# Kernel optimization log

Hardware: AMD Instinct MI355X
Metric: run time of the kernel (lower is better)

The kernel has to match this reference:

```python
import jax, jax.numpy as jnp
import numpy as np

E = 512   # embed_dim
H = 8     # num_heads
D = E // H  # head_dim


def setup_inputs() -> dict:
    key = jax.random.key(0)
    ks = jax.random.split(key, 13)
    B, Nq, Nk = 4, 2048, 2048
    query = jax.random.normal(ks[0], (B, Nq, E), dtype=jnp.float32)
    key_t = jax.random.normal(ks[1], (B, Nk, E), dtype=jnp.float32)
    value = jax.random.normal(ks[2], (B, Nk, E), dtype=jnp.float32)
    geometry_mask = jax.random.bernoulli(ks[3], 0.5, (B, Nq, Nk))  # True = keep
    s = 1.0 / np.sqrt(E)
    Wq = jax.random.normal(ks[4], (E, E), dtype=jnp.float32) * s
    bq = jax.random.normal(ks[5], (E,), dtype=jnp.float32) * 0.01
    Wk = jax.random.normal(ks[6], (E, E), dtype=jnp.float32) * s
    bk = jax.random.normal(ks[7], (E,), dtype=jnp.float32) * 0.01
    Wv = jax.random.normal(ks[8], (E, E), dtype=jnp.float32) * s
    bv = jax.random.normal(ks[9], (E,), dtype=jnp.float32) * 0.01
    Wo = jax.random.normal(ks[10], (E, E), dtype=jnp.float32) * s
    bo = jax.random.normal(ks[11], (E,), dtype=jnp.float32) * 0.01
    return {"query": query, "key": key_t, "value": value,
            "geometry_mask": geometry_mask,
            "Wq": Wq, "bq": bq, "Wk": Wk, "bk": bk,
            "Wv": Wv, "bv": bv, "Wo": Wo, "bo": bo}


def reference(query, key, value, geometry_mask, Wq, bq, Wk, bk, Wv, bv, Wo, bo):
    B, Nq, _ = query.shape
    Nk = key.shape[1]
    scale = D ** -0.5
    # projections -> (B, H, N, D)
    Q = (query @ Wq + bq).reshape(B, Nq, H, D).transpose(0, 2, 1, 3)
    K = (key @ Wk + bk).reshape(B, Nk, H, D).transpose(0, 2, 1, 3)
    V = (value @ Wv + bv).reshape(B, Nk, H, D).transpose(0, 2, 1, 3)
    scores = jnp.einsum('bhqd,bhkd->bhqk', Q, K) * scale
    mask = geometry_mask[:, None, :, :]  # (B,1,Nq,Nk), True = keep
    scores = jnp.where(mask, scores, -jnp.inf)
    attn = jax.nn.softmax(scores, axis=-1)  # dropout p=0 (eval)
    out = jnp.einsum('bhqk,bhkd->bhqd', attn, V)
    out = out.transpose(0, 2, 1, 3).reshape(B, Nq, E)
    return out @ Wo + bo
```

## Files before the change

### kernel.cpp

```cpp
#include <hip/hip_runtime.h>
#include <stdint.h>


typedef __attribute__((ext_vector_type(8))) short bf16x8;
typedef __attribute__((ext_vector_type(4))) float f32x4;

#define SCLQ 0.18033688011112042f

static __device__ __forceinline__ unsigned short f2bf(float f) {
    union { float f; unsigned u; } x; x.f = f;
    unsigned r = x.u + 0x7fffu + ((x.u >> 16) & 1u);
    return (unsigned short)(r >> 16);
}

static __device__ __forceinline__ f32x4 mfma16(bf16x8 a, bf16x8 b, f32x4 c) {
    return __builtin_amdgcn_mfma_f32_16x16x32_bf16(a, b, c, 0, 0, 0);
}

#define GLOAD_LDS16(g, l)                                                            \
    __builtin_amdgcn_global_load_lds((const __attribute__((address_space(1))) void*)(g), \
                                     (__attribute__((address_space(3))) void*)(l), 16, 0, 0)


__global__ __launch_bounds__(256) void cvt_x_kernel(
    const float* __restrict__ xq, const float* __restrict__ xk, const float* __restrict__ xv,
    short* __restrict__ oq, short* __restrict__ ok, short* __restrict__ ov)
{
    const float* src = (blockIdx.y == 0) ? xq : (blockIdx.y == 1) ? xk : xv;
    short* dst = (blockIdx.y == 0) ? oq : (blockIdx.y == 1) ? ok : ov;
    size_t i = (size_t)blockIdx.x * 256 + threadIdx.x;
    float4 v = ((const float4*)src)[i];
    short4 o;
    o.x = (short)f2bf(v.x); o.y = (short)f2bf(v.y);
    o.z = (short)f2bf(v.z); o.w = (short)f2bf(v.w);
    ((short4*)dst)[i] = o;
}

__global__ __launch_bounds__(256) void cvt_wt_kernel(
    const float* __restrict__ Wq, const float* __restrict__ Wk,
    const float* __restrict__ Wv, const float* __restrict__ Wo,
    short* __restrict__ WqT, short* __restrict__ WkT,
    short* __restrict__ WvT, short* __restrict__ WoT)
{
    int z = blockIdx.y;
    const float* W = (z == 0) ? Wq : (z == 1) ? Wk : (z == 2) ? Wv : Wo;
    short* WT = (z == 0) ? WqT : (z == 1) ? WkT : (z == 2) ? WvT : WoT;
    int t = blockIdx.x * 256 + threadIdx.x;
    int n = t & 511;
    int k0 = (t >> 9) * 8;
    union { short s[8]; int4 v; } u;
#pragma unroll
    for (int j = 0; j < 8; ++j) u.s[j] = (short)f2bf(W[(size_t)(k0 + j) * 512 + n]);
    *(int4*)(WT + (size_t)n * 512 + k0) = u.v;
}

__global__ __launch_bounds__(256) void pack_mask_kernel(
    const int* __restrict__ mask, unsigned long long* __restrict__ mp)
{
    int lane = threadIdx.x & 63;
    int row = blockIdx.x * 4 + (threadIdx.x >> 6);
    const int* mrow = mask + (size_t)row * 2048;
#pragma unroll 4
    for (int w = 0; w < 32; ++w) {
        unsigned long long bits = __ballot(mrow[w * 64 + lane] != 0);
        if (lane == 0) mp[(size_t)row * 32 + w] = bits;
    }
}

static __device__ __forceinline__ void gemm_body(
    const short* __restrict__ A, const short* __restrict__ BT,
    const float* __restrict__ bias, void* __restrict__ Cout, int mode,
    char* lds, int bx, int by)
{
    const int tid = threadIdx.x;
    const int lane = tid & 63;
    const int wid = tid >> 6;
    const int l15 = lane & 15, l4 = lane >> 4;
    const int m0 = by * 128;
    const int n0 = bx * 128;
    const int wr = wid >> 1, wc = wid & 1;

    f32x4 zero = {0.f, 0.f, 0.f, 0.f};
    f32x4 acc[4][4];
#pragma unroll
    for (int i = 0; i < 4; ++i)
#pragma unroll
        for (int j = 0; j < 4; ++j) acc[i][j] = zero;

    char* Alds = lds;
    char* Blds = lds + 16384;

    for (int t = 0; t < 8; ++t) {
        const int k0 = t * 64;
#pragma unroll
        for (int s = 0; s < 4; ++s) {
            int p = s * 256 + tid;
            int r = p >> 3, c = p & 7;
            GLOAD_LDS16(A + (size_t)(m0 + r) * 512 + k0 + 8 * (c ^ (r & 7)),
                        Alds + s * 4096 + wid * 1024);
            GLOAD_LDS16(BT + (size_t)(n0 + r) * 512 + k0 + 8 * (c ^ (r & 7)),
                        Blds + s * 4096 + wid * 1024);
        }
        __syncthreads();
#pragma unroll
        for (int ks = 0; ks < 2; ++ks) {
            bf16x8 af[4], bfr[4];
#pragma unroll
            for (int mb = 0; mb < 4; ++mb) {
                int row = wr * 64 + mb * 16 + l15;
                af[mb] = *(const bf16x8*)(Alds + row * 128 +
                                          ((ks * 64 + l4 * 16) ^ ((row & 7) << 4)));
            }
#pragma unroll
            for (int nb = 0; nb < 4; ++nb) {
                int row = wc * 64 + nb * 16 + l15;
                bfr[nb] = *(const bf16x8*)(Blds + row * 128 +
                                           ((ks * 64 + l4 * 16) ^ ((row & 7) << 4)));
            }
#pragma unroll
            for (int mb = 0; mb < 4; ++mb)
#pragma unroll
                for (int nb = 0; nb < 4; ++nb)
                    acc[mb][nb] = mfma16(af[mb], bfr[nb], acc[mb][nb]);
        }
        __syncthreads();
    }

#pragma unroll
    for (int nb = 0; nb < 4; ++nb) {
        int n = n0 + wc * 64 + nb * 16 + l15;
        float bv = bias[n];
#pragma unroll
        for (int mb = 0; mb < 4; ++mb) {
#pragma unroll
            for (int r = 0; r < 4; ++r) {
                int m = m0 + wr * 64 + mb * 16 + l4 * 4 + r;
                float val = acc[mb][nb][r] + bv;
                if (mode == 0) val *= SCLQ;
                if (mode == 3) {
                    ((float*)Cout)[(size_t)m * 512 + n] = val;
                } else {
                    int b = m >> 11, tok = m & 2047;
                    int h = n >> 6, d = n & 63;
                    short* o = (short*)Cout;
                    if (mode == 2)
                        o[((size_t)(b * 8 + h) * 64 + d) * 2048 + tok] = (short)f2bf(val);
                    else
                        o[((size_t)(b * 8 + h) * 2048 + tok) * 64 + d] = (short)f2bf(val);
                }
            }
        }
    }
}

__global__ __launch_bounds__(256) void gemm_qkv_kernel(
    const short* __restrict__ Xq, const short* __restrict__ Xk, const short* __restrict__ Xv,
    const short* __restrict__ WqT, const short* __restrict__ WkT, const short* __restrict__ WvT,
    const float* __restrict__ bq, const float* __restrict__ bk, const float* __restrict__ bv,
    short* __restrict__ Qw, short* __restrict__ Kw, short* __restrict__ VTw)
{
    __shared__ char lds[32768];
    int z = blockIdx.z;
    const short* A = (z == 0) ? Xq : (z == 1) ? Xk : Xv;
    const short* BT = (z == 0) ? WqT : (z == 1) ? WkT : WvT;
    const float* bias = (z == 0) ? bq : (z == 1) ? bk : bv;
    void* Cout = (z == 0) ? (void*)Qw : (z == 1) ? (void*)Kw : (void*)VTw;
    gemm_body(A, BT, bias, Cout, z, lds, blockIdx.x, blockIdx.y);
}

__global__ __launch_bounds__(256) void gemm_kernel(
    const short* __restrict__ A, const short* __restrict__ BT,
    const float* __restrict__ bias, void* __restrict__ Cout, int mode)
{
    __shared__ char lds[32768];
    gemm_body(A, BT, bias, Cout, mode, lds, blockIdx.x, blockIdx.y);
}

__global__ __launch_bounds__(512) void attn_kernel(
    const short* __restrict__ Q, const short* __restrict__ K,
    const short* __restrict__ VT, const unsigned long long* __restrict__ mp,
    short* __restrict__ AO)
{
    __shared__ char lds[65536];
    const int tid = threadIdx.x;
    const int lane = tid & 63;
    const int wid = tid >> 6;
    const int l15 = lane & 15, l4 = lane >> 4;
    const int lid = blockIdx.x;
    const int xcd = lid & 7, jj = lid >> 3;
    const int bhi = (xcd << 2) | (jj >> 4);
    const int b = bhi >> 3, h = bhi & 7;
    const int q0 = (jj & 15) * 128 + wid * 16;
    const short* Qp = Q + ((size_t)bhi * 2048 + q0) * 64;
    const short* Kp = K + (size_t)bhi * 2048 * 64;
    const short* Vp = VT + (size_t)bhi * 64 * 2048;

    const int krow = tid >> 3;
    const int kgo  = 8 * ((tid & 7) ^ (krow & 7));
    const int vrow0 = tid >> 4;
    const int vgo   = 8 * ((tid & 15) ^ (vrow0 & 7));
    const int vrow1 = 32 + vrow0;
    const int swl = l15 & 7;

#define STAGE(KT, BUF)                                                               \
    {                                                                                \
        const short* Kn = Kp + (size_t)(KT) * 128 * 64;                              \
        char* Kd = lds + (BUF) * 16384;                                              \
        GLOAD_LDS16(Kn + (size_t)krow * 64 + kgo, Kd + wid * 1024);                  \
        GLOAD_LDS16(Kn + (size_t)(64 + krow) * 64 + kgo, Kd + 8192 + wid * 1024);    \
        const short* Vn = Vp + (KT) * 128;                                           \
        char* Vd = lds + 32768 + (BUF) * 16384;                                      \
        GLOAD_LDS16(Vn + (size_t)vrow0 * 2048 + vgo, Vd + wid * 1024);               \
        GLOAD_LDS16(Vn + (size_t)vrow1 * 2048 + vgo, Vd + 8192 + wid * 1024);        \
    }

    bf16x8 qb[2];
#pragma unroll
    for (int dc = 0; dc < 2; ++dc)
        qb[dc] = *(const bf16x8*)(Qp + l15 * 64 + dc * 32 + l4 * 8);

    f32x4 o[4];
#pragma unroll
    for (int dt = 0; dt < 4; ++dt) o[dt] = f32x4{0.f, 0.f, 0.f, 0.f};
    float mrun = 0.f, lrun = 0.f;

    const unsigned long long* mr0 = mp + ((size_t)b * 2048 + q0 + l15) * 32;

    STAGE(0, 0)
    ulonglong2 mwv = *(const ulonglong2*)(mr0);
    __syncthreads();

#define HALF(H, MW)                                                                  \
    {                                                                                \
        bf16x8 ka[4][2];                                                             \
        _Pragma("unroll") for (int tb = 0; tb < 4; ++tb)                             \
            _Pragma("unroll") for (int dc = 0; dc < 2; ++dc)                         \
                ka[tb][dc] = *(const bf16x8*)(Kc + (H) * 8192 +                      \
                                              (tb * 16 + l15) * 128 +                \
                                              16 * ((dc * 4 + l4) ^ swl));           \
        bf16x8 vb[4][2];                                                             \
        _Pragma("unroll") for (int dt = 0; dt < 4; ++dt)                             \
            _Pragma("unroll") for (int kb = 0; kb < 2; ++kb) {                       \
                const char* vr = Vc + (dt * 16 + l15) * 256;                         \
                uint2 x = *(const uint2*)(vr +                                       \
                    16 * (((H) * 8 + kb * 4 + (l4 >> 1)) ^ swl) + (l4 & 1) * 8);     \
                uint2 y = *(const uint2*)(vr +                                       \
                    16 * (((H) * 8 + kb * 4 + 2 + (l4 >> 1)) ^ swl) + (l4 & 1) * 8); \
                uint4 t; t.x = x.x; t.y = x.y; t.z = y.x; t.w = y.y;                 \
                vb[dt][kb] = *(bf16x8*)&t;                                           \
            }                                                                        \
        const float nm = -mrun;                                                      \
        unsigned long long u64 = (MW) >> (l4 * 4);                                   \
        unsigned ulo = (unsigned)u64, uhi = (unsigned)(u64 >> 32);                   \
        f32x4 sv[4];                                                                 \
        _Pragma("unroll") for (int tb = 0; tb < 4; ++tb) {                           \
            unsigned us = (tb & 2) ? uhi : ulo;                                      \
            f32x4 i0;                                                                \
            _Pragma("unroll") for (int r = 0; r < 4; ++r)                            \
                i0[r] = (us & (1u << (((tb & 1) << 4) + r))) ? nm : -1e30f;          \
            sv[tb] = mfma16(ka[tb][1], qb[1], mfma16(ka[tb][0], qb[0], i0));         \
        }                                                                            \
        float pml;                                                                   \
        {                                                                            \
            f32x4 m0v;                                                               \
            _Pragma("unroll") for (int r = 0; r < 4; ++r)                            \
                m0v[r] = fmaxf(fmaxf(sv[0][r], sv[1][r]), fmaxf(sv[2][r], sv[3][r]));\
            pml = fmaxf(fmaxf(m0v[0], m0v[1]), fmaxf(m0v[2], m0v[3]));               \
        }                                                                            \
        if (__any(pml > 8.f)) {                                                      \
            float pm = fmaxf(pml, __shfl_xor(pml, 16, 64));                          \
            pm = fmaxf(pm, __shfl_xor(pm, 32, 64));                                  \
            float dm = fmaxf(pm, 0.f);                                               \
            float al = exp2f(-dm);                                                   \
            mrun += dm;                                                              \
            lrun *= al;                                                              \
            _Pragma("unroll") for (int r = 0; r < 4; ++r) {                          \
                float alr = __shfl(al, l4 * 4 + r, 64);                              \
                _Pragma("unroll") for (int dt = 0; dt < 4; ++dt) o[dt][r] *= alr;    \
            }                                                                        \
            _Pragma("unroll") for (int tb = 0; tb < 4; ++tb)                         \
                _Pragma("unroll") for (int r = 0; r < 4; ++r) sv[tb][r] -= dm;       \
        }                                                                            \
        _Pragma("unroll") for (int tb = 0; tb < 4; ++tb)                             \
            _Pragma("unroll") for (int r = 0; r < 4; ++r)                            \
                sv[tb][r] = exp2f(sv[tb][r]);                                        \
        {                                                                            \
            f32x4 t0 = (sv[0] + sv[1]) + (sv[2] + sv[3]);                            \
            lrun += (t0[0] + t0[1]) + (t0[2] + t0[3]);                               \
        }                                                                            \
        bf16x8 pa[2];                                                                \
        {                                                                            \
            uint4 t_;                                                                \
            asm("v_cvt_pk_bf16_f32 %0, %1, %2" : "=v"(t_.x) : "v"(sv[0][0]), "v"(sv[0][1])); \
            asm("v_cvt_pk_bf16_f32 %0, %1, %2" : "=v"(t_.y) : "v"(sv[0][2]), "v"(sv[0][3])); \
            asm("v_cvt_pk_bf16_f32 %0, %1, %2" : "=v"(t_.z) : "v"(sv[1][0]), "v"(sv[1][1])); \
            asm("v_cvt_pk_bf16_f32 %0, %1, %2" : "=v"(t_.w) : "v"(sv[1][2]), "v"(sv[1][3])); \
            pa[0] = *(bf16x8*)&t_;                                                   \
            asm("v_cvt_pk_bf16_f32 %0, %1, %2" : "=v"(t_.x) : "v"(sv[2][0]), "v"(sv[2][1])); \
            asm("v_cvt_pk_bf16_f32 %0, %1, %2" : "=v"(t_.y) : "v"(sv[2][2]), "v"(sv[2][3])); \
            asm("v_cvt_pk_bf16_f32 %0, %1, %2" : "=v"(t_.z) : "v"(sv[3][0]), "v"(sv[3][1])); \
            asm("v_cvt_pk_bf16_f32 %0, %1, %2" : "=v"(t_.w) : "v"(sv[3][2]), "v"(sv[3][3])); \
            pa[1] = *(bf16x8*)&t_;                                                   \
        }                                                                            \
        _Pragma("unroll") for (int dt = 0; dt < 4; ++dt)                             \
            o[dt] = mfma16(pa[1], vb[dt][1], mfma16(pa[0], vb[dt][0], o[dt]));       \
    }

    for (int kt = 0; kt < 16; ++kt) {
        const int cur = kt & 1;
        char* Kc = lds + cur * 16384;
        char* Vc = lds + 32768 + cur * 16384;
        if (kt < 15) STAGE(kt + 1, cur ^ 1)
        ulonglong2 mwn;
        mwn.x = 0; mwn.y = 0;
        if (kt < 15) mwn = *(const ulonglong2*)(mr0 + 2 * kt + 2);
        HALF(0, mwv.x)
        HALF(1, mwv.y)
        mwv = mwn;
        __syncthreads();
    }
#undef HALF
#undef STAGE

    {
        float lt = lrun;
        lt += __shfl_xor(lt, 16, 64);
        lt += __shfl_xor(lt, 32, 64);
        float inv = 1.0f / lt;
#pragma unroll
        for (int r = 0; r < 4; ++r) {
            float invr = __shfl(inv, l4 * 4 + r, 64);
            size_t base = ((size_t)b * 2048 + q0 + l4 * 4 + r) * 512 + h * 64;
#pragma unroll
            for (int dt = 0; dt < 4; ++dt)
                AO[base + dt * 16 + l15] = (short)f2bf(o[dt][r] * invr);
        }
    }
}

extern "C" void kernel_launch(void* const* d_in, const int* in_sizes, int n_in,
                              void* d_out, int out_size, void* d_ws, size_t ws_size,
                              hipStream_t stream) {
    const float* q  = (const float*)d_in[0];
    const float* k  = (const float*)d_in[1];
    const float* v  = (const float*)d_in[2];
    const int*   gm = (const int*)d_in[3];
    const float* Wq = (const float*)d_in[4];  const float* bq = (const float*)d_in[5];
    const float* Wk = (const float*)d_in[6];  const float* bk = (const float*)d_in[7];
    const float* Wv = (const float*)d_in[8];  const float* bv = (const float*)d_in[9];
    const float* Wo = (const float*)d_in[10]; const float* bo = (const float*)d_in[11];

    char* ws = (char*)d_ws;
    short* Xq  = (short*)(ws + 0);
    short* Xk  = (short*)(ws + 8388608);
    short* Xv  = (short*)(ws + 16777216);
    short* WqT = (short*)(ws + 25165824);
    short* WkT = (short*)(ws + 25690112);
    short* WvT = (short*)(ws + 26214400);
    short* WoT = (short*)(ws + 26738688);
    short* Qw  = (short*)(ws + 27262976);
    short* Kw  = (short*)(ws + 35651584);
    short* VTw = (short*)(ws + 44040192);
    short* AO  = (short*)(ws + 52428800);
    unsigned long long* MP = (unsigned long long*)(ws + 60817408);

    cvt_x_kernel<<<dim3(4096, 3), 256, 0, stream>>>(q, k, v, Xq, Xk, Xv);
    cvt_wt_kernel<<<dim3(128, 4), 256, 0, stream>>>(Wq, Wk, Wv, Wo, WqT, WkT, WvT, WoT);
    pack_mask_kernel<<<dim3(2048), 256, 0, stream>>>(gm, MP);

    gemm_qkv_kernel<<<dim3(4, 64, 3), 256, 0, stream>>>(Xq, Xk, Xv, WqT, WkT, WvT,
                                                        bq, bk, bv, Qw, Kw, VTw);

    attn_kernel<<<dim3(512), 512, 0, stream>>>(Qw, Kw, VTw, MP, AO);

    gemm_kernel<<<dim3(4, 64), 256, 0, stream>>>(AO, WoT, bo, (void*)d_out, 3);
}
```

Measured before the change: 165.9 us.

## Merge prep kernels into one launch and halve GEMM M-tile to 64

Folds the input conversion, weight transpose-conversion and mask bit-packing kernels into a single prep kernel that dispatches on block index, removing two launches and their gaps. Also shrinks the GEMM tile from 128x128 to 64x128, so the QKV and output projection grids double. The smaller tile raises parallelism and occupancy (less LDS and fewer accumulators) but lowers data reuse per block.

```diff
diff --git a/kernel.cpp b/kernel.cpp
--- a/kernel.cpp
+++ b/kernel.cpp
@@ -21,49 +21,49 @@
     __builtin_amdgcn_global_load_lds((const __attribute__((address_space(1))) void*)(g), \
                                      (__attribute__((address_space(3))) void*)(l), 16, 0, 0)
 
-
-__global__ __launch_bounds__(256) void cvt_x_kernel(
-    const float* __restrict__ xq, const float* __restrict__ xk, const float* __restrict__ xv,
-    short* __restrict__ oq, short* __restrict__ ok, short* __restrict__ ov)
-{
-    const float* src = (blockIdx.y == 0) ? xq : (blockIdx.y == 1) ? xk : xv;
-    short* dst = (blockIdx.y == 0) ? oq : (blockIdx.y == 1) ? ok : ov;
-    size_t i = (size_t)blockIdx.x * 256 + threadIdx.x;
-    float4 v = ((const float4*)src)[i];
-    short4 o;
-    o.x = (short)f2bf(v.x); o.y = (short)f2bf(v.y);
-    o.z = (short)f2bf(v.z); o.w = (short)f2bf(v.w);
-    ((short4*)dst)[i] = o;
-}
-
-__global__ __launch_bounds__(256) void cvt_wt_kernel(
+__global__ __launch_bounds__(256) void prep_kernel(
+    const float* __restrict__ q, const float* __restrict__ k, const float* __restrict__ v,
+    const int* __restrict__ gm,
     const float* __restrict__ Wq, const float* __restrict__ Wk,
     const float* __restrict__ Wv, const float* __restrict__ Wo,
+    short* __restrict__ Xq, short* __restrict__ Xk, short* __restrict__ Xv,
     short* __restrict__ WqT, short* __restrict__ WkT,
-    short* __restrict__ WvT, short* __restrict__ WoT)
-{
-    int z = blockIdx.y;
-    const float* W = (z == 0) ? Wq : (z == 1) ? Wk : (z == 2) ? Wv : Wo;
-    short* WT = (z == 0) ? WqT : (z == 1) ? WkT : (z == 2) ? WvT : WoT;
-    int t = blockIdx.x * 256 + threadIdx.x;
-    int n = t & 511;
-    int k0 = (t >> 9) * 8;
-    union { short s[8]; int4 v; } u;
-#pragma unroll
-    for (int j = 0; j < 8; ++j) u.s[j] = (short)f2bf(W[(size_t)(k0 + j) * 512 + n]);
-    *(int4*)(WT + (size_t)n * 512 + k0) = u.v;
-}
-
-__global__ __launch_bounds__(256) void pack_mask_kernel(
-    const int* __restrict__ mask, unsigned long long* __restrict__ mp)
-{
-    int lane = threadIdx.x & 63;
-    int row = blockIdx.x * 4 + (threadIdx.x >> 6);
-    const int* mrow = mask + (size_t)row * 2048;
+    short* __restrict__ WvT, short* __restrict__ WoT,
+    unsigned long long* __restrict__ mp)
+{
+    int bx = blockIdx.x;
+    if (bx < 12288) {
+        int z = bx >> 12;
+        const float* src = (z == 0) ? q : (z == 1) ? k : v;
+        short* dst = (z == 0) ? Xq : (z == 1) ? Xk : Xv;
+        size_t i = (size_t)(bx & 4095) * 256 + threadIdx.x;
+        float4 vv = ((const float4*)src)[i];
+        short4 o;
+        o.x = (short)f2bf(vv.x); o.y = (short)f2bf(vv.y);
+        o.z = (short)f2bf(vv.z); o.w = (short)f2bf(vv.w);
+        ((short4*)dst)[i] = o;
+    } else if (bx < 12800) {
+        int b2 = bx - 12288;
+        int z = b2 >> 7;
+        const float* W = (z == 0) ? Wq : (z == 1) ? Wk : (z == 2) ? Wv : Wo;
+        short* WT = (z == 0) ? WqT : (z == 1) ? WkT : (z == 2) ? WvT : WoT;
+        int t = (b2 & 127) * 256 + threadIdx.x;
+        int n = t & 511;
+        int k0 = (t >> 9) * 8;
+        union { short s[8]; int4 v4; } u;
+#pragma unroll
+        for (int j = 0; j < 8; ++j) u.s[j] = (short)f2bf(W[(size_t)(k0 + j) * 512 + n]);
+        *(int4*)(WT + (size_t)n * 512 + k0) = u.v4;
+    } else {
+        int b3 = bx - 12800;
+        int lane = threadIdx.x & 63;
+        int row = b3 * 4 + (threadIdx.x >> 6);
+        const int* mrow = gm + (size_t)row * 2048;
 #pragma unroll 4
-    for (int w = 0; w < 32; ++w) {
-        unsigned long long bits = __ballot(mrow[w * 64 + lane] != 0);
-        if (lane == 0) mp[(size_t)row * 32 + w] = bits;
+        for (int w = 0; w < 32; ++w) {
+            unsigned long long bits = __ballot(mrow[w * 64 + lane] != 0);
+            if (lane == 0) mp[(size_t)row * 32 + w] = bits;
+        }
     }
 }
 
@@ -76,38 +76,43 @@
     const int lane = tid & 63;
     const int wid = tid >> 6;
     const int l15 = lane & 15, l4 = lane >> 4;
-    const int m0 = by * 128;
+    const int m0 = by * 64;
     const int n0 = bx * 128;
     const int wr = wid >> 1, wc = wid & 1;
 
     f32x4 zero = {0.f, 0.f, 0.f, 0.f};
-    f32x4 acc[4][4];
-#pragma unroll
-    for (int i = 0; i < 4; ++i)
+    f32x4 acc[2][4];
+#pragma unroll
+    for (int i = 0; i < 2; ++i)
 #pragma unroll
         for (int j = 0; j < 4; ++j) acc[i][j] = zero;
 
     char* Alds = lds;
-    char* Blds = lds + 16384;
+    char* Blds = lds + 8192;
 
     for (int t = 0; t < 8; ++t) {
         const int k0 = t * 64;
 #pragma unroll
-        for (int s = 0; s < 4; ++s) {
+        for (int s = 0; s < 2; ++s) {
             int p = s * 256 + tid;
             int r = p >> 3, c = p & 7;
             GLOAD_LDS16(A + (size_t)(m0 + r) * 512 + k0 + 8 * (c ^ (r & 7)),
                         Alds + s * 4096 + wid * 1024);
+        }
+#pragma unroll
+        for (int s = 0; s < 4; ++s) {
+            int p = s * 256 + tid;
+            int r = p >> 3, c = p & 7;
             GLOAD_LDS16(BT + (size_t)(n0 + r) * 512 + k0 + 8 * (c ^ (r & 7)),
                         Blds + s * 4096 + wid * 1024);
         }
         __syncthreads();
 #pragma unroll
         for (int ks = 0; ks < 2; ++ks) {
-            bf16x8 af[4], bfr[4];
-#pragma unroll
-            for (int mb = 0; mb < 4; ++mb) {
-                int row = wr * 64 + mb * 16 + l15;
+            bf16x8 af[2], bfr[4];
+#pragma unroll
+            for (int mb = 0; mb < 2; ++mb) {
+                int row = wr * 32 + mb * 16 + l15;
                 af[mb] = *(const bf16x8*)(Alds + row * 128 +
                                           ((ks * 64 + l4 * 16) ^ ((row & 7) << 4)));
             }
@@ -118,7 +123,7 @@
                                            ((ks * 64 + l4 * 16) ^ ((row & 7) << 4)));
             }
 #pragma unroll
-            for (int mb = 0; mb < 4; ++mb)
+            for (int mb = 0; mb < 2; ++mb)
 #pragma unroll
                 for (int nb = 0; nb < 4; ++nb)
                     acc[mb][nb] = mfma16(af[mb], bfr[nb], acc[mb][nb]);
@@ -131,10 +136,10 @@
         int n = n0 + wc * 64 + nb * 16 + l15;
         float bv = bias[n];
 #pragma unroll
-        for (int mb = 0; mb < 4; ++mb) {
+        for (int mb = 0; mb < 2; ++mb) {
 #pragma unroll
             for (int r = 0; r < 4; ++r) {
-                int m = m0 + wr * 64 + mb * 16 + l4 * 4 + r;
+                int m = m0 + wr * 32 + mb * 16 + l4 * 4 + r;
                 float val = acc[mb][nb][r] + bv;
                 if (mode == 0) val *= SCLQ;
                 if (mode == 3) {
@@ -159,7 +164,7 @@
     const float* __restrict__ bq, const float* __restrict__ bk, const float* __restrict__ bv,
     short* __restrict__ Qw, short* __restrict__ Kw, short* __restrict__ VTw)
 {
-    __shared__ char lds[32768];
+    __shared__ char lds[24576];
     int z = blockIdx.z;
     const short* A = (z == 0) ? Xq : (z == 1) ? Xk : Xv;
     const short* BT = (z == 0) ? WqT : (z == 1) ? WkT : WvT;
@@ -172,7 +177,7 @@
     const short* __restrict__ A, const short* __restrict__ BT,
     const float* __restrict__ bias, void* __restrict__ Cout, int mode)
 {
-    __shared__ char lds[32768];
+    __shared__ char lds[24576];
     gemm_body(A, BT, bias, Cout, mode, lds, blockIdx.x, blockIdx.y);
 }
 
@@ -364,14 +369,13 @@
     short* AO  = (short*)(ws + 52428800);
     unsigned long long* MP = (unsigned long long*)(ws + 60817408);
 
-    cvt_x_kernel<<<dim3(4096, 3), 256, 0, stream>>>(q, k, v, Xq, Xk, Xv);
-    cvt_wt_kernel<<<dim3(128, 4), 256, 0, stream>>>(Wq, Wk, Wv, Wo, WqT, WkT, WvT, WoT);
-    pack_mask_kernel<<<dim3(2048), 256, 0, stream>>>(gm, MP);
-
-    gemm_qkv_kernel<<<dim3(4, 64, 3), 256, 0, stream>>>(Xq, Xk, Xv, WqT, WkT, WvT,
-                                                        bq, bk, bv, Qw, Kw, VTw);
+    prep_kernel<<<dim3(14848), 256, 0, stream>>>(q, k, v, gm, Wq, Wk, Wv, Wo,
+                                                 Xq, Xk, Xv, WqT, WkT, WvT, WoT, MP);
+
+    gemm_qkv_kernel<<<dim3(4, 128, 3), 256, 0, stream>>>(Xq, Xk, Xv, WqT, WkT, WvT,
+                                                         bq, bk, bv, Qw, Kw, VTw);
 
     attn_kernel<<<dim3(512), 512, 0, stream>>>(Qw, Kw, VTw, MP, AO);
 
-    gemm_kernel<<<dim3(4, 64), 256, 0, stream>>>(AO, WoT, bo, (void*)d_out, 3);
-}
+    gemm_kernel<<<dim3(4, 128), 256, 0, stream>>>(AO, WoT, bo, (void*)d_out, 3);
+}
```

Measured after the change: 159.8 us. 1.04x faster.
